# Performance work log

Measured on AMD Instinct MI355X. Metric: run time of the kernel, lower is better.

Reference implementation:

```python
import jax, jax.numpy as jnp
import numpy as np

NEG_SLOPE = 0.2
EPS = 1e-5

N_NODES = 50000
N_GRAPHS = 500
NODES_PER_GRAPH = 100
N_EDGES = 500000
F_IN = 16
F_GRAPH = 4
HID = 64
N_CLASSES = 2


def setup_inputs() -> dict:
    key = jax.random.key(0)
    ks = jax.random.split(key, 32)
    x = jax.random.normal(ks[0], (N_NODES, F_IN), dtype=jnp.float32)
    # intra-graph random edges: dst lives in the same 100-node block as src
    src = jax.random.randint(ks[1], (N_EDGES,), 0, N_NODES)
    dst = (src // NODES_PER_GRAPH) * NODES_PER_GRAPH + jax.random.randint(ks[2], (N_EDGES,), 0, NODES_PER_GRAPH)
    edge_index = jnp.stack([src, dst]).astype(jnp.int64)
    graph_input = jax.random.normal(ks[3], (N_GRAPHS, F_GRAPH), dtype=jnp.float32)
    batch = (jnp.arange(N_NODES) // NODES_PER_GRAPH).astype(jnp.int64)

    def w(k, shape, scale=0.1):
        return (jax.random.normal(k, shape, dtype=jnp.float32) * scale)

    inp = dict(x=x, edge_index=edge_index, graph_input=graph_input, batch=batch)
    # GraphNorm params
    inp['gn_w'] = jnp.ones((F_IN,), jnp.float32)
    inp['gn_b'] = w(ks[4], (F_IN,))
    inp['gn_ms'] = jnp.ones((F_IN,), jnp.float32)
    inp['W1'] = w(ks[5], (F_IN, 4 * HID))
    inp['as1'] = w(ks[6], (4, HID)); inp['ad1'] = w(ks[7], (4, HID))
    inp['b1'] = w(ks[8], (4 * HID,))
    inp['W2'] = w(ks[9], (4 * HID, 4 * HID))
    inp['as2'] = w(ks[10], (4, HID)); inp['ad2'] = w(ks[11], (4, HID))
    inp['b2'] = w(ks[12], (4 * HID,))
    inp['W3'] = w(ks[13], (4 * HID, HID))
    inp['as3'] = w(ks[14], (1, HID)); inp['ad3'] = w(ks[15], (1, HID))
    inp['b3'] = w(ks[16], (HID,))
    # BatchNorm1d (eval mode) over [HID + F_GRAPH]
    D = HID + F_GRAPH
    inp['bn_g'] = 1.0 + w(ks[17], (D,))
    inp['bn_b'] = w(ks[18], (D,))
    inp['bn_m'] = jnp.zeros((D,), jnp.float32)
    inp['bn_v'] = jnp.ones((D,), jnp.float32)
    # Dense head
    inp['Wd1'] = w(ks[19], (D, HID)); inp['bd1'] = w(ks[20], (HID,))
    inp['Wd2'] = w(ks[21], (HID, HID)); inp['bd2'] = w(ks[22], (HID,))
    inp['Wo'] = w(ks[23], (HID, N_CLASSES)); inp['bo'] = w(ks[24], (N_CLASSES,))
    return inp


def _segment_softmax(e, seg, n):
    m = jax.ops.segment_max(e, seg, num_segments=n)
    ex = jnp.exp(e - m[seg])
    s = jax.ops.segment_sum(ex, seg, num_segments=n)
    return ex / s[seg]


def _gat_conv(x, src, dst, W, att_src, att_dst, b):
    N = x.shape[0]
    H, C = att_src.shape
    loop = jnp.arange(N)
    src = jnp.concatenate([src, loop])  # PyG GATConv adds self-loops
    dst = jnp.concatenate([dst, loop])
    h = (x @ W).reshape(N, H, C)
    a_src = (h * att_src).sum(-1)  # [N,H]
    a_dst = (h * att_dst).sum(-1)
    e = jax.nn.leaky_relu(a_src[src] + a_dst[dst], NEG_SLOPE)  # [E,H]
    alpha = _segment_softmax(e, dst, N)
    out = jax.ops.segment_sum(h[src] * alpha[:, :, None], dst, num_segments=N)
    return out.reshape(N, H * C) + b


def _graph_norm(x, batch, n_graphs, w, b, ms):
    cnt = jax.ops.segment_sum(jnp.ones((x.shape[0],), x.dtype), batch, num_segments=n_graphs)[:, None]
    mean = jax.ops.segment_sum(x, batch, num_segments=n_graphs) / cnt
    out = x - mean[batch] * ms
    var = jax.ops.segment_sum(out * out, batch, num_segments=n_graphs) / cnt
    return w * out / jnp.sqrt(var[batch] + EPS) + b


def _global_mean_pool(x, batch, n_graphs):
    cnt = jax.ops.segment_sum(jnp.ones((x.shape[0],), x.dtype), batch, num_segments=n_graphs)[:, None]
    return jax.ops.segment_sum(x, batch, num_segments=n_graphs) / cnt


def reference(x, edge_index, graph_input, batch,
              gn_w, gn_b, gn_ms,
              W1, as1, ad1, b1,
              W2, as2, ad2, b2,
              W3, as3, ad3, b3,
              bn_g, bn_b, bn_m, bn_v,
              Wd1, bd1, Wd2, bd2, Wo, bo):
    src, dst = edge_index[0], edge_index[1]
    G = graph_input.shape[0]
    h = _graph_norm(x, batch, G, gn_w, gn_b, gn_ms)
    # dropout is a no-op in eval
    h = jax.nn.elu(_gat_conv(h, src, dst, W1, as1, ad1, b1))
    h = jax.nn.elu(_gat_conv(h, src, dst, W2, as2, ad2, b2))
    h = _gat_conv(h, src, dst, W3, as3, ad3, b3)
    g = _global_mean_pool(h, batch, G)
    g = jnp.concatenate([g, graph_input], axis=1)
    g = (g - bn_m) / jnp.sqrt(bn_v + EPS) * bn_g + bn_b  # BatchNorm1d eval
    g = jax.nn.selu(g @ Wd1 + bd1)
    g = jax.nn.selu(g @ Wd2 + bd2)
    g = g @ Wo + bo
    return jax.nn.softmax(g, axis=1)
```

## Files before the change

kernel.cpp:

```cpp
#include <hip/hip_runtime.h>
#include <math.h>

#define N_NODES 50000
#define N_ROWS_PAD 50048
#define N_GRAPHS 500
#define NPG 100
#define N_EDGES 500000
#define F_IN 16
#define HID 64
#define EW_CAP 1408

#define SELU_SCALE 1.0507009873554804934193349852946f
#define SELU_ALPHA 1.6732632423543772848170429916717f

typedef __attribute__((ext_vector_type(8))) short short8;
typedef __attribute__((ext_vector_type(8))) unsigned short ushort8;
typedef __attribute__((ext_vector_type(4))) float floatx4;

__device__ __forceinline__ float lrelu(float x){ return x > 0.f ? x : 0.2f * x; }
__device__ __forceinline__ float eluf(float x){ return x > 0.f ? x : expf(x) - 1.f; }
__device__ __forceinline__ float seluf(float x){
    return x > 0.f ? SELU_SCALE * x : SELU_SCALE * (SELU_ALPHA * (expf(x) - 1.f));
}
__device__ __forceinline__ unsigned short f2bf(float x){
    unsigned u = __float_as_uint(x);
    return (unsigned short)((u + 0x7FFFu + ((u >> 16) & 1u)) >> 16);
}
__device__ __forceinline__ float bf2f(unsigned short u){
    return __uint_as_float((unsigned)u << 16);
}
__device__ __forceinline__ float bf2f_lo(unsigned u){
    return __uint_as_float(u << 16);
}
__device__ __forceinline__ float bf2f_hi(unsigned u){
    return __uint_as_float(u & 0xFFFF0000u);
}

__global__ void k_count(const int* __restrict__ dst, int* __restrict__ counts){
    int e = blockIdx.x * 256 + threadIdx.x;
    if (e < N_EDGES) atomicAdd(&counts[dst[e]], 1);
}

__global__ void k_local_scan(const int* __restrict__ counts, int* __restrict__ local_off,
                             int* __restrict__ graph_tot){
    __shared__ int s[128];
    int g = blockIdx.x, t = threadIdx.x;
    int v = (t < NPG) ? counts[g * NPG + t] : 0;
    s[t] = v; __syncthreads();
    for (int o = 1; o < 128; o <<= 1){
        int x = (t >= o) ? s[t - o] : 0;
        __syncthreads();
        s[t] += x;
        __syncthreads();
    }
    if (t < NPG) local_off[g * NPG + t] = s[t] - v;
    if (t == 127) graph_tot[g] = s[127];
}

__global__ void k_graph_scan(const int* __restrict__ graph_tot, int* __restrict__ graph_base){
    __shared__ int s[512];
    int t = threadIdx.x;
    int v = (t < N_GRAPHS) ? graph_tot[t] : 0;
    s[t] = v; __syncthreads();
    for (int o = 1; o < 512; o <<= 1){
        int x = (t >= o) ? s[t - o] : 0;
        __syncthreads();
        s[t] += x;
        __syncthreads();
    }
    if (t < N_GRAPHS) graph_base[t] = s[t] - v;
}

__global__ void k_off(const int* __restrict__ local_off, const int* __restrict__ graph_base,
                      int* __restrict__ node_off, int* __restrict__ write_ptr){
    int n = blockIdx.x * 256 + threadIdx.x;
    if (n < N_NODES){
        int v = local_off[n] + graph_base[n / NPG];
        node_off[n] = v;
        write_ptr[n] = v;
    }
}

__global__ void k_scatter(const int* __restrict__ src, const int* __restrict__ dst,
                          int* __restrict__ write_ptr, int* __restrict__ csr){
    int e = blockIdx.x * 256 + threadIdx.x;
    if (e < N_EDGES){
        int d = dst[e];
        int pos = atomicAdd(&write_ptr[d], 1);
        int b = (d / NPG) * NPG;
        csr[pos] = (src[e] - b) | ((d - b) << 8);
    }
}

__global__ void k_gnorm(const float* __restrict__ x, const float* __restrict__ w,
                        const float* __restrict__ b, const float* __restrict__ ms,
                        float* __restrict__ y){
    __shared__ float sx[NPG * F_IN];
    __shared__ float red[16][16];
    __shared__ float meanS[16], varS[16];
    int g = blockIdx.x, t = threadIdx.x;
    for (int idx = t; idx < NPG * F_IN; idx += 256) sx[idx] = x[g * NPG * F_IN + idx];
    __syncthreads();
    int f = t & 15, grp = t >> 4;
    float p = 0.f;
    for (int i = grp; i < NPG; i += 16) p += sx[i * 16 + f];
    red[grp][f] = p; __syncthreads();
    if (t < 16){
        float s = 0.f;
        for (int i = 0; i < 16; i++) s += red[i][t];
        meanS[t] = s * (1.f / 100.f);
    }
    __syncthreads();
    float mm = meanS[f] * ms[f];
    p = 0.f;
    for (int i = grp; i < NPG; i += 16){ float v = sx[i * 16 + f] - mm; p += v * v; }
    red[grp][f] = p; __syncthreads();
    if (t < 16){
        float s = 0.f;
        for (int i = 0; i < 16; i++) s += red[i][t];
        varS[t] = s * (1.f / 100.f);
    }
    __syncthreads();
    for (int idx = t; idx < NPG * F_IN; idx += 256){
        int ff = idx & 15;
        float v = sx[idx] - meanS[ff] * ms[ff];
        y[g * NPG * F_IN + idx] = w[ff] * v * rsqrtf(varS[ff] + 1e-5f) + b[ff];
    }
}

__global__ void k_gemm_tiled(const float* __restrict__ X, const float* __restrict__ W,
                             unsigned short* __restrict__ Ybf, int N, int K, int OUT){
    __shared__ float As[16][68];
    __shared__ float Bs[16][68];
    int t = threadIdx.x;
    int r0 = blockIdx.y * 64;
    int c0 = blockIdx.x * 64;
    int tx = t & 15, ty = t >> 4;
    float acc[4][4];
    #pragma unroll
    for (int i = 0; i < 4; i++)
        #pragma unroll
        for (int j = 0; j < 4; j++) acc[i][j] = 0.f;

    int lk = t & 15;
    int lm0 = t >> 4;
    int ln = t & 63;
    int lkb = t >> 6;

    for (int kt = 0; kt < K; kt += 16){
        #pragma unroll
        for (int i = 0; i < 4; i++){
            int m = lm0 + i * 16;
            int row = r0 + m;
            As[lk][m] = (row < N) ? X[row * K + kt + lk] : 0.f;
        }
        #pragma unroll
        for (int i = 0; i < 4; i++){
            int k = lkb + i * 4;
            Bs[k][ln] = W[(kt + k) * OUT + c0 + ln];
        }
        __syncthreads();
        #pragma unroll
        for (int k = 0; k < 16; k++){
            float4 a = *(const float4*)&As[k][ty * 4];
            float4 b = *(const float4*)&Bs[k][tx * 4];
            float av[4] = {a.x, a.y, a.z, a.w};
            float bv[4] = {b.x, b.y, b.z, b.w};
            #pragma unroll
            for (int i = 0; i < 4; i++)
                #pragma unroll
                for (int j = 0; j < 4; j++) acc[i][j] += av[i] * bv[j];
        }
        __syncthreads();
    }
    int hh = c0 >> 6;
    #pragma unroll
    for (int i = 0; i < 4; i++){
        int row = r0 + ty * 4 + i;
        if (row < N){
            #pragma unroll
            for (int j = 0; j < 4; j++)
                Ybf[(size_t)row * 256 + (tx * 4 + j) * 4 + hh] = f2bf(acc[i][j]);
        }
    }
}

__global__ void k_pack_w(const float* __restrict__ W, unsigned short* __restrict__ Wp,
                         int K, int OUT){
    int idx = blockIdx.x * 256 + threadIdx.x;
    if (idx >= K * OUT) return;
    int k = idx / OUT, n = idx - k * OUT;
    Wp[(((k >> 3) * OUT) + n) * 8 + (k & 7)] = f2bf(W[idx]);
}

__global__ void k_gemm_mfma(const unsigned short* __restrict__ Xb,
                            const unsigned short* __restrict__ Wp,
                            unsigned short* __restrict__ Ybf,
                            int N, int K, int OUT, int interleave){
    int t = threadIdx.x;
    int wave = t >> 6, lane = t & 63;
    int quad = lane >> 4, ln = lane & 15;
    int r0 = blockIdx.y * 64 + wave * 16;
    int c0 = blockIdx.x * 64;

    floatx4 acc[4];
    #pragma unroll
    for (int f = 0; f < 4; f++) acc[f] = (floatx4){0.f, 0.f, 0.f, 0.f};

    const unsigned short* aptr = Xb + (size_t)(r0 + ln) * K + quad * 8;
    for (int kt = 0; kt < K; kt += 32){
        short8 a = *(const short8*)(aptr + kt);
        int kc = (kt >> 3) + quad;
        #pragma unroll
        for (int f = 0; f < 4; f++){
            short8 b = *(const short8*)(Wp + ((size_t)kc * OUT + c0 + f * 16 + ln) * 8);
            acc[f] = __builtin_amdgcn_mfma_f32_16x16x32_bf16(a, b, acc[f], 0, 0, 0);
        }
    }
    int rowb = r0 + quad * 4;
    if (interleave){
        int hh = c0 >> 6;
        #pragma unroll
        for (int f = 0; f < 4; f++){
            int c = f * 16 + ln;
            #pragma unroll
            for (int rg = 0; rg < 4; rg++){
                int row = rowb + rg;
                if (row < N) Ybf[(size_t)row * 256 + c * 4 + hh] = f2bf(acc[f][rg]);
            }
        }
    } else {
        #pragma unroll
        for (int f = 0; f < 4; f++){
            int col = c0 + f * 16 + ln;
            #pragma unroll
            for (int rg = 0; rg < 4; rg++){
                int row = rowb + rg;
                if (row < N) Ybf[(size_t)row * OUT + col] = f2bf(acc[f][rg]);
            }
        }
    }
}

__global__ void __launch_bounds__(512)
k_fused4(const unsigned short* __restrict__ hbf, const float* __restrict__ as,
         const float* __restrict__ ad, const float* __restrict__ bias,
         const int* __restrict__ csr, const int* __restrict__ noff,
         const int* __restrict__ cnt, unsigned short* __restrict__ out_bf){
    __shared__ __align__(16) unsigned short hl[NPG * 256];
    __shared__ __align__(16) unsigned int edl[EW_CAP][4];
    __shared__ __align__(16) float asrcl[NPG * 4], adstl[NPG * 4];
    __shared__ __align__(16) float wselfl[NPG * 4], rsuml[NPG * 4];
    __shared__ int offl[NPG], cntl[NPG];

    int g = blockIdx.x, t = threadIdx.x;
    int wave = t >> 6, lane = t & 63;
    int base = g * NPG;

    int ebeg = noff[base];
    int etot = noff[base + NPG - 1] + cnt[base + NPG - 1] - ebeg;
    int eln = etot < EW_CAP ? etot : EW_CAP;

    const ushort8* hsrc = (const ushort8*)(hbf + (size_t)base * 256);
    for (int i = t; i < NPG * 32; i += 512) ((ushort8*)hl)[i] = hsrc[i];
    for (int i = t; i < eln; i += 512) edl[i][2] = (unsigned)csr[ebeg + i];
    if (t < NPG){ offl[t] = noff[base + t]; cntl[t] = cnt[base + t]; }
    __syncthreads();

    {
        int cl = lane & 15, nsub = lane >> 4;
        float av[4][4], dv[4][4];
        #pragma unroll
        for (int hh = 0; hh < 4; hh++){
            float4 a4 = *(const float4*)&as[hh * 64 + cl * 4];
            float4 d4 = *(const float4*)&ad[hh * 64 + cl * 4];
            av[hh][0] = a4.x; av[hh][1] = a4.y; av[hh][2] = a4.z; av[hh][3] = a4.w;
            dv[hh][0] = d4.x; dv[hh][1] = d4.y; dv[hh][2] = d4.z; dv[hh][3] = d4.w;
        }
        for (int g0 = wave * 4; g0 < NPG; g0 += 32){
            int n = g0 + nsub;
            ushort8 lo = *(const ushort8*)&hl[n * 256 + cl * 16];
            ushort8 hi = *(const ushort8*)&hl[n * 256 + cl * 16 + 8];
            float ps[4] = {0.f, 0.f, 0.f, 0.f}, pd[4] = {0.f, 0.f, 0.f, 0.f};
            #pragma unroll
            for (int k = 0; k < 2; k++){
                #pragma unroll
                for (int hh = 0; hh < 4; hh++){
                    float x = bf2f(lo[k * 4 + hh]);
                    ps[hh] = fmaf(x, av[hh][k], ps[hh]);
                    pd[hh] = fmaf(x, dv[hh][k], pd[hh]);
                }
            }
            #pragma unroll
            for (int k = 0; k < 2; k++){
                #pragma unroll
                for (int hh = 0; hh < 4; hh++){
                    float x = bf2f(hi[k * 4 + hh]);
                    ps[hh] = fmaf(x, av[hh][k + 2], ps[hh]);
                    pd[hh] = fmaf(x, dv[hh][k + 2], pd[hh]);
                }
            }
            #pragma unroll
            for (int o = 8; o >= 1; o >>= 1){
                #pragma unroll
                for (int hh = 0; hh < 4; hh++){
                    ps[hh] += __shfl_xor(ps[hh], o);
                    pd[hh] += __shfl_xor(pd[hh], o);
                }
            }
            if (cl == 0){
                *(float4*)&asrcl[n * 4] = make_float4(ps[0], ps[1], ps[2], ps[3]);
                *(float4*)&adstl[n * 4] = make_float4(pd[0], pd[1], pd[2], pd[3]);
            }
        }
    }
    __syncthreads();

    for (int i = t; i < eln; i += 512){
        unsigned sd = edl[i][2];
        int s = sd & 0xFF, d = sd >> 8;
        float4 av = *(const float4*)&asrcl[s * 4];
        float4 dv = *(const float4*)&adstl[d * 4];
        unsigned w0 = f2bf(expf(lrelu(av.x + dv.x)));
        unsigned w1 = f2bf(expf(lrelu(av.y + dv.y)));
        unsigned w2 = f2bf(expf(lrelu(av.z + dv.z)));
        unsigned w3 = f2bf(expf(lrelu(av.w + dv.w)));
        edl[i][0] = w0 | (w1 << 16);
        edl[i][1] = w2 | (w3 << 16);
    }
    __syncthreads();

    if (t < NPG){
        int d = t;
        float4 av = *(const float4*)&asrcl[d * 4];
        float4 dv = *(const float4*)&adstl[d * 4];
        float ws0 = expf(lrelu(av.x + dv.x));
        float ws1 = expf(lrelu(av.y + dv.y));
        float ws2 = expf(lrelu(av.z + dv.z));
        float ws3 = expf(lrelu(av.w + dv.w));
        float s0 = ws0, s1 = ws1, s2 = ws2, s3 = ws3;
        int ebg = offl[d] - ebeg, n = cntl[d];
        for (int j = 0; j < n; j++){
            uint2 v = *(const uint2*)&edl[ebg + j][0];
            s0 += bf2f_lo(v.x); s1 += bf2f_hi(v.x);
            s2 += bf2f_lo(v.y); s3 += bf2f_hi(v.y);
        }
        *(float4*)&wselfl[d * 4] = make_float4(ws0, ws1, ws2, ws3);
        *(float4*)&rsuml[d * 4]  = make_float4(1.f / s0, 1.f / s1, 1.f / s2, 1.f / s3);
    }
    __syncthreads();

    float b0 = bias[lane], b1 = bias[64 + lane], b2 = bias[128 + lane], b3 = bias[192 + lane];
    for (int d = wave; d < NPG; d += 8){
        float4 ws = *(const float4*)&wselfl[d * 4];
        float4 rs = *(const float4*)&rsuml[d * 4];
        ushort4 hv = *(const ushort4*)&hl[d * 256 + lane * 4];
        float a0 = ws.x * bf2f(hv.x);
        float a1 = ws.y * bf2f(hv.y);
        float a2 = ws.z * bf2f(hv.z);
        float a3 = ws.w * bf2f(hv.w);
        int ebg = offl[d] - ebeg, n = cntl[d];
        int j = 0;
        #pragma unroll 1
        for (; j + 4 <= n; j += 4){
            #pragma unroll
            for (int k = 0; k < 4; k++){
                uint4 v = *(const uint4*)&edl[ebg + j + k][0];
                int s = (int)(v.z & 0xFFu);
                ushort4 x = *(const ushort4*)&hl[s * 256 + lane * 4];
                a0 = fmaf(bf2f_lo(v.x), bf2f(x.x), a0);
                a1 = fmaf(bf2f_hi(v.x), bf2f(x.y), a1);
                a2 = fmaf(bf2f_lo(v.y), bf2f(x.z), a2);
                a3 = fmaf(bf2f_hi(v.y), bf2f(x.w), a3);
            }
        }
        for (; j < n; j++){
            uint4 v = *(const uint4*)&edl[ebg + j][0];
            int s = (int)(v.z & 0xFFu);
            ushort4 x = *(const ushort4*)&hl[s * 256 + lane * 4];
            a0 = fmaf(bf2f_lo(v.x), bf2f(x.x), a0);
            a1 = fmaf(bf2f_hi(v.x), bf2f(x.y), a1);
            a2 = fmaf(bf2f_lo(v.y), bf2f(x.z), a2);
            a3 = fmaf(bf2f_hi(v.y), bf2f(x.w), a3);
        }
        size_t ob = (size_t)(base + d) * 256 + lane;
        out_bf[ob]       = f2bf(eluf(a0 * rs.x + b0));
        out_bf[ob + 64]  = f2bf(eluf(a1 * rs.y + b1));
        out_bf[ob + 128] = f2bf(eluf(a2 * rs.z + b2));
        out_bf[ob + 192] = f2bf(eluf(a3 * rs.w + b3));
    }
}

__global__ void __launch_bounds__(256)
k_fused1(const unsigned short* __restrict__ hbf, const float* __restrict__ as,
         const float* __restrict__ ad, const float* __restrict__ bias,
         const int* __restrict__ csr, const int* __restrict__ noff,
         const int* __restrict__ cnt, float* __restrict__ out){
    __shared__ __align__(16) unsigned short hl[NPG * 64];
    __shared__ __align__(16) unsigned int edl[EW_CAP][2];
    __shared__ float asrcl[NPG], adstl[NPG];
    __shared__ float wselfl[NPG], rsuml[NPG];
    __shared__ int offl[NPG], cntl[NPG];

    int g = blockIdx.x, t = threadIdx.x;
    int wave = t >> 6, lane = t & 63;
    int base = g * NPG;

    int ebeg = noff[base];
    int etot = noff[base + NPG - 1] + cnt[base + NPG - 1] - ebeg;
    int eln = etot < EW_CAP ? etot : EW_CAP;

    const ushort8* hsrc = (const ushort8*)(hbf + (size_t)base * 64);
    for (int i = t; i < NPG * 8; i += 256) ((ushort8*)hl)[i] = hsrc[i];
    for (int i = t; i < eln; i += 256) edl[i][1] = (unsigned)csr[ebeg + i];
    if (t < NPG){ offl[t] = noff[base + t]; cntl[t] = cnt[base + t]; }
    __syncthreads();

    {
        int cl = lane & 15, nsub = lane >> 4;
        float4 a4 = *(const float4*)&as[cl * 4];
        float4 d4 = *(const float4*)&ad[cl * 4];
        for (int g0 = wave * 4; g0 < NPG; g0 += 16){
            int n = g0 + nsub;
            ushort4 u = *(const ushort4*)&hl[n * 64 + cl * 4];
            float x0 = bf2f(u.x), x1 = bf2f(u.y), x2 = bf2f(u.z), x3 = bf2f(u.w);
            float ps = x0 * a4.x + x1 * a4.y + x2 * a4.z + x3 * a4.w;
            float pd = x0 * d4.x + x1 * d4.y + x2 * d4.z + x3 * d4.w;
            #pragma unroll
            for (int o = 8; o >= 1; o >>= 1){
                ps += __shfl_xor(ps, o);
                pd += __shfl_xor(pd, o);
            }
            if (cl == 0){ asrcl[n] = ps; adstl[n] = pd; }
        }
    }
    __syncthreads();

    for (int i = t; i < eln; i += 256){
        unsigned sd = edl[i][1];
        int s = sd & 0xFF, d = sd >> 8;
        edl[i][0] = (unsigned)f2bf(expf(lrelu(asrcl[s] + adstl[d])));
    }
    __syncthreads();

    if (t < NPG){
        float wsf = expf(lrelu(asrcl[t] + adstl[t]));
        float sum = wsf;
        int ebg = offl[t] - ebeg, n = cntl[t];
        for (int j = 0; j < n; j++) sum += bf2f((unsigned short)edl[ebg + j][0]);
        wselfl[t] = wsf;
        rsuml[t] = 1.f / sum;
    }
    __syncthreads();

    float bl = bias[lane];
    for (int d = wave; d < NPG; d += 4){
        float acc = wselfl[d] * bf2f(hl[d * 64 + lane]);
        int ebg = offl[d] - ebeg, n = cntl[d];
        for (int j = 0; j < n; j++){
            uint2 v = *(const uint2*)&edl[ebg + j][0];
            acc = fmaf(bf2f_lo(v.x), bf2f(hl[(int)(v.y & 0xFFu) * 64 + lane]), acc);
        }
        out[(size_t)(base + d) * 64 + lane] = acc * rsuml[d] + bl;
    }
}

__global__ void k_head(const float* __restrict__ x3, const float* __restrict__ gin,
                       const float* __restrict__ bn_g, const float* __restrict__ bn_b,
                       const float* __restrict__ bn_m, const float* __restrict__ bn_v,
                       const float* __restrict__ Wd1, const float* __restrict__ bd1,
                       const float* __restrict__ Wd2, const float* __restrict__ bd2,
                       const float* __restrict__ Wo, const float* __restrict__ bo,
                       float* __restrict__ out){
    __shared__ float red[256];
    __shared__ float gv[68];
    __shared__ float g2[64];
    __shared__ float g3[64];
    int g = blockIdx.x, t = threadIdx.x;
    int c = t & 63, grp = t >> 6;
    float p = 0.f;
    for (int i = grp; i < NPG; i += 4) p += x3[(g * NPG + i) * 64 + c];
    red[t] = p; __syncthreads();
    if (t < 64){
        float s = red[t] + red[t + 64] + red[t + 128] + red[t + 192];
        float mean = s * (1.f / 100.f);
        gv[t] = (mean - bn_m[t]) * rsqrtf(bn_v[t] + 1e-5f) * bn_g[t] + bn_b[t];
    } else if (t < 68){
        int j = t - 64;
        float v = gin[g * 4 + j];
        gv[t] = (v - bn_m[t]) * rsqrtf(bn_v[t] + 1e-5f) * bn_g[t] + bn_b[t];
    }
    __syncthreads();
    if (t < 64){
        float s = bd1[t];
        for (int i = 0; i < 68; i++) s += gv[i] * Wd1[i * 64 + t];
        g2[t] = seluf(s);
    }
    __syncthreads();
    if (t < 64){
        float s = bd2[t];
        for (int i = 0; i < 64; i++) s += g2[i] * Wd2[i * 64 + t];
        g3[t] = seluf(s);
    }
    __syncthreads();
    if (t == 0){
        float l0 = bo[0], l1 = bo[1];
        for (int i = 0; i < 64; i++){ l0 += g3[i] * Wo[i * 2]; l1 += g3[i] * Wo[i * 2 + 1]; }
        float mx = fmaxf(l0, l1);
        float e0 = expf(l0 - mx), e1 = expf(l1 - mx);
        float inv = 1.f / (e0 + e1);
        out[g * 2] = e0 * inv;
        out[g * 2 + 1] = e1 * inv;
    }
}

extern "C" void kernel_launch(void* const* d_in, const int* in_sizes, int n_in,
                              void* d_out, int out_size, void* d_ws, size_t ws_size,
                              hipStream_t stream){
    const float* x   = (const float*)d_in[0];
    const int*   ei  = (const int*)d_in[1];
    const float* gin = (const float*)d_in[2];
    const float* gn_w = (const float*)d_in[4];
    const float* gn_b = (const float*)d_in[5];
    const float* gn_ms = (const float*)d_in[6];
    const float* W1 = (const float*)d_in[7];
    const float* as1 = (const float*)d_in[8];
    const float* ad1 = (const float*)d_in[9];
    const float* b1 = (const float*)d_in[10];
    const float* W2 = (const float*)d_in[11];
    const float* as2 = (const float*)d_in[12];
    const float* ad2 = (const float*)d_in[13];
    const float* b2 = (const float*)d_in[14];
    const float* W3 = (const float*)d_in[15];
    const float* as3 = (const float*)d_in[16];
    const float* ad3 = (const float*)d_in[17];
    const float* b3 = (const float*)d_in[18];
    const float* bn_g = (const float*)d_in[19];
    const float* bn_b = (const float*)d_in[20];
    const float* bn_m = (const float*)d_in[21];
    const float* bn_v = (const float*)d_in[22];
    const float* Wd1 = (const float*)d_in[23];
    const float* bd1 = (const float*)d_in[24];
    const float* Wd2 = (const float*)d_in[25];
    const float* bd2 = (const float*)d_in[26];
    const float* Wo = (const float*)d_in[27];
    const float* bo = (const float*)d_in[28];
    float* out = (float*)d_out;

    const int* src = ei;
    const int* dst = ei + N_EDGES;

    char* ws = (char*)d_ws;
    size_t off = 0;
    auto alloc = [&](size_t bytes) -> void* {
        void* p = ws + off;
        off = (off + bytes + 255) & ~(size_t)255;
        return p;
    };
    int* counts     = (int*)alloc((size_t)N_NODES * 4);
    int* local_off  = (int*)alloc((size_t)N_NODES * 4);
    int* node_off   = (int*)alloc((size_t)N_NODES * 4);
    int* write_ptr  = (int*)alloc((size_t)N_NODES * 4);
    int* graph_tot  = (int*)alloc(512 * 4);
    int* graph_base = (int*)alloc(512 * 4);
    int* csr        = (int*)alloc((size_t)N_EDGES * 4);
    float* y        = (float*)alloc((size_t)N_NODES * F_IN * 4);
    unsigned short* wp2 = (unsigned short*)alloc((size_t)256 * 256 * 2);
    unsigned short* wp3 = (unsigned short*)alloc((size_t)256 * 64 * 2);
    unsigned short* xbh = (unsigned short*)alloc((size_t)N_NODES * 256 * 2);
    unsigned short* xb  = (unsigned short*)alloc((size_t)N_ROWS_PAD * 256 * 2);
    unsigned short* x3b = (unsigned short*)alloc((size_t)N_NODES * HID * 2);
    float* bufD     = (float*)alloc((size_t)N_NODES * HID * 4);

    hipMemsetAsync(counts, 0, (size_t)N_NODES * 4, stream);
    k_count<<<(N_EDGES + 255) / 256, 256, 0, stream>>>(dst, counts);
    k_local_scan<<<N_GRAPHS, 128, 0, stream>>>(counts, local_off, graph_tot);
    k_graph_scan<<<1, 512, 0, stream>>>(graph_tot, graph_base);
    k_off<<<(N_NODES + 255) / 256, 256, 0, stream>>>(local_off, graph_base, node_off, write_ptr);
    k_scatter<<<(N_EDGES + 255) / 256, 256, 0, stream>>>(src, dst, write_ptr, csr);

    k_pack_w<<<(256 * 256 + 255) / 256, 256, 0, stream>>>(W2, wp2, 256, 256);
    k_pack_w<<<(256 * 64 + 255) / 256, 256, 0, stream>>>(W3, wp3, 256, 64);

    k_gnorm<<<N_GRAPHS, 256, 0, stream>>>(x, gn_w, gn_b, gn_ms, y);

    dim3 gemm_grid4(4, (N_NODES + 63) / 64);
    dim3 mfma_grid4(4, N_ROWS_PAD / 64);
    dim3 mfma_grid1(1, N_ROWS_PAD / 64);

    k_gemm_tiled<<<gemm_grid4, 256, 0, stream>>>(y, W1, xbh, N_NODES, 16, 256);
    k_fused4<<<N_GRAPHS, 512, 0, stream>>>(xbh, as1, ad1, b1, csr, node_off, counts, xb);

    k_gemm_mfma<<<mfma_grid4, 256, 0, stream>>>(xb, wp2, xbh, N_NODES, 256, 256, 1);
    k_fused4<<<N_GRAPHS, 512, 0, stream>>>(xbh, as2, ad2, b2, csr, node_off, counts, xb);

    k_gemm_mfma<<<mfma_grid1, 256, 0, stream>>>(xb, wp3, x3b, N_NODES, 256, 64, 0);
    k_fused1<<<N_GRAPHS, 256, 0, stream>>>(x3b, as3, ad3, b3, csr, node_off, counts, bufD);

    k_head<<<N_GRAPHS, 256, 0, stream>>>(bufD, gin, bn_g, bn_b, bn_m, bn_v,
                                         Wd1, bd1, Wd2, bd2, Wo, bo, out);
}
```

Baseline: 381.7 us.

## Restructure node-feature GEMMs for full-width tiles and vectorized interleaved stores

The first-layer fp32 GEMM now has each block compute all 256 output columns for 64 rows with the whole W1 held in shared memory, instead of four column-tiled blocks. The MFMA GEMM is templated on output width and swaps operands so each lane owns one node row, covering every column in one block. This lets the head-interleaved bf16 output be written with 16-byte vector stores instead of scattered 2-byte stores, and it avoids re-reading X across column blocks. In exchange each thread holds more accumulators (64 floats in the tiled kernel, 16 MFMA accumulators), which raises register pressure and may lower occupancy.

```diff
diff --git a/kernel.cpp b/kernel.cpp
--- a/kernel.cpp
+++ b/kernel.cpp
@@ -128,59 +128,58 @@
     }
 }
 
-__global__ void k_gemm_tiled(const float* __restrict__ X, const float* __restrict__ W,
-                             unsigned short* __restrict__ Ybf, int N, int K, int OUT){
-    __shared__ float As[16][68];
-    __shared__ float Bs[16][68];
+__global__ void __launch_bounds__(256)
+k_gemm_tiled(const float* __restrict__ X, const float* __restrict__ W,
+             unsigned short* __restrict__ Ybf, int N){
+    __shared__ float As[64][17];
+    __shared__ float Bs[16][256];
     int t = threadIdx.x;
-    int r0 = blockIdx.y * 64;
-    int c0 = blockIdx.x * 64;
-    int tx = t & 15, ty = t >> 4;
-    float acc[4][4];
+    int r0 = blockIdx.x * 64;
+    {
+        int row = t >> 2, kq = t & 3;
+        float4 v = (r0 + row < N) ? *(const float4*)&X[(size_t)(r0 + row) * 16 + kq * 4]
+                                  : make_float4(0.f, 0.f, 0.f, 0.f);
+        As[row][kq * 4 + 0] = v.x; As[row][kq * 4 + 1] = v.y;
+        As[row][kq * 4 + 2] = v.z; As[row][kq * 4 + 3] = v.w;
+    }
+    for (int i = t; i < 1024; i += 256)
+        *(float4*)&Bs[0][i * 4] = *(const float4*)&W[i * 4];
+    __syncthreads();
+
+    int c4 = t & 15, rsub = t >> 4;
+    float acc[4][16];
     #pragma unroll
     for (int i = 0; i < 4; i++)
         #pragma unroll
-        for (int j = 0; j < 4; j++) acc[i][j] = 0.f;
-
-    int lk = t & 15;
-    int lm0 = t >> 4;
-    int ln = t & 63;
-    int lkb = t >> 6;
-
-    for (int kt = 0; kt < K; kt += 16){
-        #pragma unroll
-        for (int i = 0; i < 4; i++){
-            int m = lm0 + i * 16;
-            int row = r0 + m;
-            As[lk][m] = (row < N) ? X[row * K + kt + lk] : 0.f;
-        }
-        #pragma unroll
-        for (int i = 0; i < 4; i++){
-            int k = lkb + i * 4;
-            Bs[k][ln] = W[(kt + k) * OUT + c0 + ln];
-        }
-        __syncthreads();
-        #pragma unroll
-        for (int k = 0; k < 16; k++){
-            float4 a = *(const float4*)&As[k][ty * 4];
-            float4 b = *(const float4*)&Bs[k][tx * 4];
-            float av[4] = {a.x, a.y, a.z, a.w};
-            float bv[4] = {b.x, b.y, b.z, b.w};
-            #pragma unroll
-            for (int i = 0; i < 4; i++)
-                #pragma unroll
-                for (int j = 0; j < 4; j++) acc[i][j] += av[i] * bv[j];
-        }
-        __syncthreads();
-    }
-    int hh = c0 >> 6;
+        for (int j = 0; j < 16; j++) acc[i][j] = 0.f;
+
+    for (int k = 0; k < 16; k++){
+        float a_[4];
+        #pragma unroll
+        for (int i = 0; i < 4; i++) a_[i] = As[rsub + 16 * i][k];
+        float4 b0 = *(const float4*)&Bs[k][c4 * 4];
+        float4 b1 = *(const float4*)&Bs[k][64 + c4 * 4];
+        float4 b2 = *(const float4*)&Bs[k][128 + c4 * 4];
+        float4 b3 = *(const float4*)&Bs[k][192 + c4 * 4];
+        float bv[16] = {b0.x, b0.y, b0.z, b0.w, b1.x, b1.y, b1.z, b1.w,
+                        b2.x, b2.y, b2.z, b2.w, b3.x, b3.y, b3.z, b3.w};
+        #pragma unroll
+        for (int i = 0; i < 4; i++)
+            #pragma unroll
+            for (int j = 0; j < 16; j++) acc[i][j] = fmaf(a_[i], bv[j], acc[i][j]);
+    }
     #pragma unroll
     for (int i = 0; i < 4; i++){
-        int row = r0 + ty * 4 + i;
+        int row = r0 + rsub + 16 * i;
         if (row < N){
-            #pragma unroll
-            for (int j = 0; j < 4; j++)
-                Ybf[(size_t)row * 256 + (tx * 4 + j) * 4 + hh] = f2bf(acc[i][j]);
+            ushort8 ua, ub;
+            #pragma unroll
+            for (int m = 0; m < 8; m++){
+                ua[m] = f2bf(acc[i][(m & 3) * 4 + (m >> 2)]);
+                ub[m] = f2bf(acc[i][(m & 3) * 4 + 2 + (m >> 2)]);
+            }
+            *(ushort8*)&Ybf[(size_t)row * 256 + c4 * 16]     = ua;
+            *(ushort8*)&Ybf[(size_t)row * 256 + c4 * 16 + 8] = ub;
         }
     }
 }
@@ -193,51 +192,58 @@
     Wp[(((k >> 3) * OUT) + n) * 8 + (k & 7)] = f2bf(W[idx]);
 }
 
-__global__ void k_gemm_mfma(const unsigned short* __restrict__ Xb,
-                            const unsigned short* __restrict__ Wp,
-                            unsigned short* __restrict__ Ybf,
-                            int N, int K, int OUT, int interleave){
+template<int OUT, int ILV>
+__global__ void __launch_bounds__(256)
+k_gemm_mfma(const unsigned short* __restrict__ Xb,
+            const unsigned short* __restrict__ Wp,
+            unsigned short* __restrict__ Ybf, int N, int K){
+    const int NF = OUT / 16;
     int t = threadIdx.x;
     int wave = t >> 6, lane = t & 63;
     int quad = lane >> 4, ln = lane & 15;
-    int r0 = blockIdx.y * 64 + wave * 16;
-    int c0 = blockIdx.x * 64;
-
-    floatx4 acc[4];
+    int node = blockIdx.x * 64 + wave * 16 + ln;
+
+    floatx4 acc[NF];
     #pragma unroll
-    for (int f = 0; f < 4; f++) acc[f] = (floatx4){0.f, 0.f, 0.f, 0.f};
-
-    const unsigned short* aptr = Xb + (size_t)(r0 + ln) * K + quad * 8;
+    for (int f = 0; f < NF; f++) acc[f] = (floatx4){0.f, 0.f, 0.f, 0.f};
+
+    const unsigned short* bptr = Xb + (size_t)node * K + quad * 8;
     for (int kt = 0; kt < K; kt += 32){
-        short8 a = *(const short8*)(aptr + kt);
+        short8 b = *(const short8*)(bptr + kt);
         int kc = (kt >> 3) + quad;
         #pragma unroll
-        for (int f = 0; f < 4; f++){
-            short8 b = *(const short8*)(Wp + ((size_t)kc * OUT + c0 + f * 16 + ln) * 8);
+        for (int f = 0; f < NF; f++){
+            short8 a = *(const short8*)(Wp + ((size_t)kc * OUT + f * 16 + ln) * 8);
             acc[f] = __builtin_amdgcn_mfma_f32_16x16x32_bf16(a, b, acc[f], 0, 0, 0);
         }
     }
-    int rowb = r0 + quad * 4;
-    if (interleave){
-        int hh = c0 >> 6;
-        #pragma unroll
-        for (int f = 0; f < 4; f++){
-            int c = f * 16 + ln;
-            #pragma unroll
-            for (int rg = 0; rg < 4; rg++){
-                int row = rowb + rg;
-                if (row < N) Ybf[(size_t)row * 256 + c * 4 + hh] = f2bf(acc[f][rg]);
+    if (node >= N) return;
+
+    if (ILV){
+        unsigned short h[NF][4];
+        #pragma unroll
+        for (int f = 0; f < NF; f++)
+            #pragma unroll
+            for (int r = 0; r < 4; r++) h[f][r] = f2bf(acc[f][r]);
+        #pragma unroll
+        for (int f0 = 0; f0 < 4; f0++){
+            #pragma unroll
+            for (int rp = 0; rp < 2; rp++){
+                ushort8 u;
+                u[0] = h[f0][2 * rp];      u[1] = h[f0 + 4][2 * rp];
+                u[2] = h[f0 + 8][2 * rp];  u[3] = h[f0 + 12][2 * rp];
+                u[4] = h[f0][2 * rp + 1];  u[5] = h[f0 + 4][2 * rp + 1];
+                u[6] = h[f0 + 8][2 * rp + 1]; u[7] = h[f0 + 12][2 * rp + 1];
+                *(ushort8*)&Ybf[(size_t)node * 256 + f0 * 64 + quad * 16 + rp * 8] = u;
             }
         }
     } else {
         #pragma unroll
-        for (int f = 0; f < 4; f++){
-            int col = c0 + f * 16 + ln;
-            #pragma unroll
-            for (int rg = 0; rg < 4; rg++){
-                int row = rowb + rg;
-                if (row < N) Ybf[(size_t)row * OUT + col] = f2bf(acc[f][rg]);
-            }
+        for (int f = 0; f < NF; f++){
+            ushort4 u;
+            u.x = f2bf(acc[f][0]); u.y = f2bf(acc[f][1]);
+            u.z = f2bf(acc[f][2]); u.w = f2bf(acc[f][3]);
+            *(ushort4*)&Ybf[(size_t)node * OUT + f * 16 + quad * 4] = u;
         }
     }
 }
@@ -584,17 +590,13 @@
 
     k_gnorm<<<N_GRAPHS, 256, 0, stream>>>(x, gn_w, gn_b, gn_ms, y);
 
-    dim3 gemm_grid4(4, (N_NODES + 63) / 64);
-    dim3 mfma_grid4(4, N_ROWS_PAD / 64);
-    dim3 mfma_grid1(1, N_ROWS_PAD / 64);
-
-    k_gemm_tiled<<<gemm_grid4, 256, 0, stream>>>(y, W1, xbh, N_NODES, 16, 256);
+    k_gemm_tiled<<<(N_NODES + 63) / 64, 256, 0, stream>>>(y, W1, xbh, N_NODES);
     k_fused4<<<N_GRAPHS, 512, 0, stream>>>(xbh, as1, ad1, b1, csr, node_off, counts, xb);
 
-    k_gemm_mfma<<<mfma_grid4, 256, 0, stream>>>(xb, wp2, xbh, N_NODES, 256, 256, 1);
+    k_gemm_mfma<256, 1><<<N_ROWS_PAD / 64, 256, 0, stream>>>(xb, wp2, xbh, N_NODES, 256);
     k_fused4<<<N_GRAPHS, 512, 0, stream>>>(xbh, as2, ad2, b2, csr, node_off, counts, xb);
 
-    k_gemm_mfma<<<mfma_grid1, 256, 0, stream>>>(xb, wp3, x3b, N_NODES, 256, 64, 0);
+    k_gemm_mfma<64, 0><<<N_ROWS_PAD / 64, 256, 0, stream>>>(xb, wp3, x3b, N_NODES, 256);
     k_fused1<<<N_GRAPHS, 256, 0, stream>>>(x3b, as3, ad3, b3, csr, node_off, counts, bufD);
 
     k_head<<<N_GRAPHS, 256, 0, stream>>>(bufD, gin, bn_g, bn_b, bn_m, bn_v,
```

Result: slower. 407.9 us (+6.9%).
